# Performance work log

Hardware: AMD Instinct MI355X
Metric: run time of the kernel (lower is better)

Reference implementation:

```python
import jax, jax.numpy as jnp
import numpy as np
from jax import lax

B = 32      # point clouds per batch
P = 1024    # points per cloud (equal-sized, contiguous in batch vector)
K = 20      # kNN neighbors (includes self, as in PyG knn)
N = B * P


def _w(key, fan_in, fan_out):
    return jax.random.normal(key, (fan_in, fan_out), dtype=jnp.float32) / np.sqrt(fan_in)


def setup_inputs() -> dict:
    key = jax.random.key(0)
    ks = jax.random.split(key, 12)
    return {
        "pos": jax.random.normal(ks[0], (N, 3), dtype=jnp.float32),
        "batch": jnp.repeat(jnp.arange(B, dtype=jnp.int32), P),
        # conv1 MLP([6,64,64]): Linear(6,64)+BN+ReLU, Linear(64,64) plain
        "conv1_W1": _w(ks[1], 6, 64),
        "conv1_b1": jnp.zeros((64,), jnp.float32),
        "conv1_bn_scale": jnp.ones((64,), jnp.float32),   # BN eval folded affine
        "conv1_bn_bias": jnp.zeros((64,), jnp.float32),
        "conv1_W2": _w(ks[2], 64, 64),
        "conv1_b2": jnp.zeros((64,), jnp.float32),
        # conv2 MLP([128,128]): single plain Linear(128,128)
        "conv2_W": _w(ks[3], 128, 128),
        "conv2_b": jnp.zeros((128,), jnp.float32),
        # lin: Linear(64+128, 128)
        "lin_W": _w(ks[4], 192, 128),
        "lin_b": jnp.zeros((128,), jnp.float32),
    }


def _edge_conv(x, mlp_fn):
    # x: [B, P, d]. Dynamic kNN in feature space per cloud, edge MLP, max-aggregate.
    sq = jnp.sum(x * x, axis=-1)                                  # [B,P]
    dist = sq[:, :, None] - 2.0 * jnp.einsum('bpd,bqd->bpq', x, x) + sq[:, None, :]
    _, idx = lax.top_k(-dist, K)                                  # [B,P,K] nearest (incl. self)
    x_j = jax.vmap(lambda xb, ib: xb[ib])(x, idx)                 # [B,P,K,d] gather neighbors
    x_i = jnp.broadcast_to(x[:, :, None, :], x_j.shape)
    e = jnp.concatenate([x_i, x_j - x_i], axis=-1)                # [B,P,K,2d]
    return jnp.max(mlp_fn(e), axis=2)                             # max aggregation -> [B,P,out]


def reference(pos, batch, conv1_W1, conv1_b1, conv1_bn_scale, conv1_bn_bias,
              conv1_W2, conv1_b2, conv2_W, conv2_b, lin_W, lin_b):
    x = pos.reshape(B, P, 3)

    def mlp1(e):
        h = e @ conv1_W1 + conv1_b1
        h = jax.nn.relu(h * conv1_bn_scale + conv1_bn_bias)       # BN(eval) + ReLU
        return h @ conv1_W2 + conv1_b2                            # plain last layer

    def mlp2(e):
        return e @ conv2_W + conv2_b                              # plain single layer

    x1 = _edge_conv(x, mlp1)                                      # [B,P,64]
    x2 = _edge_conv(x1, mlp2)                                     # [B,P,128]
    h = jnp.concatenate([x1, x2], axis=-1) @ lin_W + lin_b        # [B,P,128]
    # global_max_pool over each cloud via batch ids
    out = jax.ops.segment_max(h.reshape(N, 128), batch, num_segments=B)
    return out                                                    # [B,128]
```

## Files before the change

kernel.cpp:

```cpp
#include <hip/hip_runtime.h>
#include <math.h>

#define NPTS 32768
#define NB 32
#define PP 1024
#define KK 20

using bf16x8 = __attribute__((ext_vector_type(8))) short;
using f32x4 = __attribute__((ext_vector_type(4))) float;

constexpr size_t OFF_X1 = 0;
constexpr size_t OFF_IDX = OFF_X1 + (size_t)NPTS * 64 * 4;
constexpr size_t OFF_U = OFF_IDX + (size_t)NPTS * KK * 4;
constexpr size_t OFF_V = OFF_U + (size_t)NPTS * 128 * 4;
constexpr size_t OFF_X2 = OFF_V + (size_t)NPTS * 128 * 4;
constexpr size_t OFF_H = OFF_X2 + (size_t)NPTS * 128 * 4;
constexpr size_t OFF_PART = OFF_H + (size_t)NPTS * 128 * 4;
constexpr size_t OFF_SQN = OFF_PART + (size_t)32 * 8 * 128 * 4;

__device__ __forceinline__ void topk_insert(unsigned (&l)[KK], unsigned key) {
#pragma unroll
  for (int j = KK - 1; j >= 1; --j) {
    unsigned r;
    asm("v_med3_u32 %0, %1, %2, %3" : "=v"(r) : "v"(key), "v"(l[j - 1]), "v"(l[j]));
    l[j] = r;
  }
  l[0] = key < l[0] ? key : l[0];
}

__device__ __forceinline__ unsigned pack_key(float dist, int q) {
  return (__float_as_uint(dist) & 0xFFFFFC00u) | (unsigned)q;
}

__device__ __forceinline__ void split_bf16(float x, short& hi, short& lo) {
  unsigned u = __float_as_uint(x);
  hi = (short)(u >> 16);
  float fh = __uint_as_float(u & 0xFFFF0000u);
  float r = x - fh;
  lo = (short)(__float_as_uint(r) >> 16);
}

template <int S>
__global__ __launch_bounds__(256, 4) void knn_topk3(const float* __restrict__ x,
                                                    unsigned* __restrict__ pk) {
  constexpr int CH = PP / S;
  __shared__ __align__(16) float xs[1024];
  __shared__ __align__(16) float ys[1024];
  __shared__ __align__(16) float zs[1024];
  int bx = blockIdx.x;
  int s = bx % S;
  int tile = (bx / S) % (PP / 256);
  int b = bx / (S * (PP / 256));
  int tid = threadIdx.x;
  const float* xb = x + (size_t)b * PP * 3;

  for (int t = tid; t < 768; t += 256) {
    float4 v = ((const float4*)xb)[t];
    int e = 4 * t;
    float vals[4] = {v.x, v.y, v.z, v.w};
#pragma unroll
    for (int j = 0; j < 4; ++j) {
      int p = (e + j) / 3, d = (e + j) % 3;
      if (d == 0) xs[p] = vals[j];
      else if (d == 1) ys[p] = vals[j];
      else zs[p] = vals[j];
    }
  }
  __syncthreads();

  int i = tile * 256 + tid;
  float xi0 = xs[i], xi1 = ys[i], xi2 = zs[i];

  unsigned l[KK];
#pragma unroll
  for (int j = 0; j < KK; ++j) l[j] = 0xFFFFFFFFu;

  int q0 = s * CH;
  float4 qx = *(const float4*)&xs[q0];
  float4 qy = *(const float4*)&ys[q0];
  float4 qz = *(const float4*)&zs[q0];
  for (int c = 0; c < CH; c += 4) {
    int qm = (q0 + c + 4) & 1023;
    float4 nqx = *(const float4*)&xs[qm];
    float4 nqy = *(const float4*)&ys[qm];
    float4 nqz = *(const float4*)&zs[qm];
    float cx[4] = {qx.x, qx.y, qx.z, qx.w};
    float cy[4] = {qy.x, qy.y, qy.z, qy.w};
    float cz[4] = {qz.x, qz.y, qz.z, qz.w};
#pragma unroll
    for (int j = 0; j < 4; ++j) {
      float d0 = xi0 - cx[j], d1 = xi1 - cy[j], d2 = xi2 - cz[j];
      float dist = fmaf(d0, d0, fmaf(d1, d1, d2 * d2));
      topk_insert(l, pack_key(dist, q0 + c + j));
    }
    qx = nqx; qy = nqy; qz = nqz;
  }
  size_t base = ((size_t)b * PP + i) * S + s;
#pragma unroll
  for (int j = 0; j < KK; ++j) pk[base * KK + j] = l[j];
}

template <int S>
__global__ __launch_bounds__(256) void knn_merge(const unsigned* __restrict__ pk,
                                                 int* __restrict__ idx_out) {
  int p = blockIdx.x * 256 + threadIdx.x;
  const unsigned* g = pk + (size_t)p * S * KK;
  unsigned l[KK];
#pragma unroll
  for (int j = 0; j < KK; ++j) l[j] = g[j];
  for (int s = 1; s < S; ++s) {
    const unsigned* gs = g + s * KK;
    for (int j = 0; j < KK; ++j) {
      unsigned key = gs[j];
      if (key >= l[KK - 1]) break;
      topk_insert(l, key);
    }
  }
#pragma unroll
  for (int j = 0; j < KK; ++j) idx_out[(size_t)p * KK + j] = (int)(l[j] & 1023u);
}

__global__ __launch_bounds__(256) void precompute1(const float* __restrict__ pos,
                                                   const float* __restrict__ W1,
                                                   const float* __restrict__ b1,
                                                   float* __restrict__ u1,
                                                   float* __restrict__ v1) {
  int gid = blockIdx.x * 256 + threadIdx.x;
  int i = gid >> 6, c = gid & 63;
  float p0 = pos[(size_t)i * 3 + 0], p1 = pos[(size_t)i * 3 + 1], p2 = pos[(size_t)i * 3 + 2];
  float a0 = W1[0 * 64 + c], a1 = W1[1 * 64 + c], a2 = W1[2 * 64 + c];
  float g0 = W1[3 * 64 + c], g1 = W1[4 * 64 + c], g2 = W1[5 * 64 + c];
  float v = fmaf(p0, g0, fmaf(p1, g1, p2 * g2));
  float u = b1[c];
  u = fmaf(p0, a0 - g0, u);
  u = fmaf(p1, a1 - g1, u);
  u = fmaf(p2, a2 - g2, u);
  u1[gid] = u;
  v1[gid] = v;
}

__global__ __launch_bounds__(256) void edge_conv1_mfma(
    const float* __restrict__ u1, const float* __restrict__ v1,
    const int* __restrict__ idx, const float* __restrict__ W2,
    const float* __restrict__ scale, const float* __restrict__ bias,
    const float* __restrict__ b2,
    short* __restrict__ x1hl, float* __restrict__ sqn) {
  __shared__ float Cs[160 * 68];
  __shared__ int jt[160];
  __shared__ float xs[512];
  int tid = threadIdx.x;
  int p0 = blockIdx.x * 8;
  int b = p0 >> 10;
  if (tid < 160) {
    int e = tid;
    int i = p0 + e / 20;
    jt[e] = (b << 10) + idx[(size_t)i * KK + e % 20];
  }
  int w = tid >> 6, l = tid & 63, quad = l >> 4, lm = l & 15;
  int kq = quad * 8;
  float4 s00 = *(const float4*)(scale + kq);
  float4 s01 = *(const float4*)(scale + kq + 4);
  float4 s10 = *(const float4*)(scale + 32 + kq);
  float4 s11 = *(const float4*)(scale + 32 + kq + 4);
  float4 c00 = *(const float4*)(bias + kq);
  float4 c01 = *(const float4*)(bias + kq + 4);
  float4 c10 = *(const float4*)(bias + 32 + kq);
  float4 c11 = *(const float4*)(bias + 32 + kq + 4);
  bf16x8 Bh[4][2], Bl[4][2];
#pragma unroll
  for (int nt = 0; nt < 4; ++nt) {
#pragma unroll
    for (int ks = 0; ks < 2; ++ks) {
#pragma unroll
      for (int jj = 0; jj < 8; ++jj) {
        float wv = W2[(size_t)(ks * 32 + kq + jj) * 64 + nt * 16 + lm];
        short hi, lo;
        split_bf16(wv, hi, lo);
        Bh[nt][ks][jj] = hi;
        Bl[nt][ks][jj] = lo;
      }
    }
  }
  __syncthreads();

  for (int s = w; s < 10; s += 4) {
    f32x4 acc[4];
#pragma unroll
    for (int nt = 0; nt < 4; ++nt) acc[nt] = (f32x4){0.f, 0.f, 0.f, 0.f};
    int e = s * 16 + lm;
    int p = e / 20;
    int jrow = jt[e];
    const float* urow = u1 + (size_t)(p0 + p) * 64;
    const float* vrow = v1 + (size_t)jrow * 64;
#pragma unroll
    for (int ks = 0; ks < 2; ++ks) {
      int koff = ks * 32 + kq;
      float4 va = *(const float4*)(vrow + koff);
      float4 vb = *(const float4*)(vrow + koff + 4);
      float4 ua = *(const float4*)(urow + koff);
      float4 ub = *(const float4*)(urow + koff + 4);
      float4 sA = ks ? s10 : s00, sB = ks ? s11 : s01;
      float4 cA = ks ? c10 : c00, cB = ks ? c11 : c01;
      float hv[8];
      hv[0] = fmaxf(fmaf(ua.x + va.x, sA.x, cA.x), 0.f);
      hv[1] = fmaxf(fmaf(ua.y + va.y, sA.y, cA.y), 0.f);
      hv[2] = fmaxf(fmaf(ua.z + va.z, sA.z, cA.z), 0.f);
      hv[3] = fmaxf(fmaf(ua.w + va.w, sA.w, cA.w), 0.f);
      hv[4] = fmaxf(fmaf(ub.x + vb.x, sB.x, cB.x), 0.f);
      hv[5] = fmaxf(fmaf(ub.y + vb.y, sB.y, cB.y), 0.f);
      hv[6] = fmaxf(fmaf(ub.z + vb.z, sB.z, cB.z), 0.f);
      hv[7] = fmaxf(fmaf(ub.w + vb.w, sB.w, cB.w), 0.f);
      bf16x8 Ah, Al;
#pragma unroll
      for (int jj = 0; jj < 8; ++jj) {
        short hi, lo;
        split_bf16(hv[jj], hi, lo);
        Ah[jj] = hi;
        Al[jj] = lo;
      }
#pragma unroll
      for (int nt = 0; nt < 4; ++nt) {
        acc[nt] = __builtin_amdgcn_mfma_f32_16x16x32_bf16(Ah, Bh[nt][ks], acc[nt], 0, 0, 0);
        acc[nt] = __builtin_amdgcn_mfma_f32_16x16x32_bf16(Al, Bh[nt][ks], acc[nt], 0, 0, 0);
        acc[nt] = __builtin_amdgcn_mfma_f32_16x16x32_bf16(Ah, Bl[nt][ks], acc[nt], 0, 0, 0);
      }
    }
#pragma unroll
    for (int nt = 0; nt < 4; ++nt) {
#pragma unroll
      for (int r = 0; r < 4; ++r) {
        Cs[(size_t)(s * 16 + quad * 4 + r) * 68 + nt * 16 + lm] = acc[nt][r];
      }
    }
  }
  __syncthreads();
  for (int o = tid; o < 512; o += 256) {
    int p = o >> 6, c = o & 63;
    float m = -__builtin_inff();
    for (int k = 0; k < KK; ++k) m = fmaxf(m, Cs[(size_t)(p * 20 + k) * 68 + c]);
    m += b2[c];
    size_t gi = (size_t)(p0 + p) * 128 + c;
    short hi, lo;
    split_bf16(m, hi, lo);
    x1hl[gi] = hi;
    x1hl[gi + 64] = lo;
    xs[o] = m;
  }
  __syncthreads();
  if (tid < 8) {
    float ss = 0.f;
    for (int c = 0; c < 64; ++c) {
      float v = xs[tid * 64 + c];
      ss = fmaf(v, v, ss);
    }
    sqn[p0 + tid] = ss;
  }
}

__global__ __launch_bounds__(256, 4) void knn2_mfma(const short* __restrict__ x1hl,
                                                    const float* __restrict__ sqn,
                                                    unsigned* __restrict__ pk) {
  constexpr int TS = 72;
  __shared__ float sqs[512];
  __shared__ __align__(16) short tileH[2][64 * TS];
  __shared__ __align__(16) short tileL[2][64 * TS];
  int bx = blockIdx.x;
  int s = bx & 1;
  int pb = bx >> 1;
  int p0 = pb * 64;
  int b = p0 >> 10;
  int tid = threadIdx.x;
  for (int t = tid; t < 512; t += 256) sqs[t] = sqn[(size_t)b * PP + s * 512 + t];
  int w = tid >> 6, l = tid & 63, quad = l >> 4, lm = l & 15;
  size_t gi = (size_t)p0 + w * 16 + lm;
  const short* brow = x1hl + gi * 128 + quad * 8;
  bf16x8 Bh0 = *(const bf16x8*)(brow);
  bf16x8 Bl0 = *(const bf16x8*)(brow + 64);
  bf16x8 Bh1 = *(const bf16x8*)(brow + 32);
  bf16x8 Bl1 = *(const bf16x8*)(brow + 96);
  float sqi = sqn[gi];

  unsigned la[KK], lc[KK];
#pragma unroll
  for (int j = 0; j < KK; ++j) { la[j] = 0xFFFFFFFFu; lc[j] = 0xFFFFFFFFu; }

  int rr = tid & 63, seg = tid >> 6;
  const short* srcbase = x1hl + ((size_t)b * PP + s * 512 + rr) * 128 + seg * 32;
  {
    bf16x8 r0 = *(const bf16x8*)(srcbase);
    bf16x8 r1 = *(const bf16x8*)(srcbase + 8);
    bf16x8 r2 = *(const bf16x8*)(srcbase + 16);
    bf16x8 r3 = *(const bf16x8*)(srcbase + 24);
    short* dst = ((seg < 2) ? tileH[0] : tileL[0]) + rr * TS + (seg & 1) * 32;
    *(bf16x8*)(dst) = r0;
    *(bf16x8*)(dst + 8) = r1;
    *(bf16x8*)(dst + 16) = r2;
    *(bf16x8*)(dst + 24) = r3;
  }
  __syncthreads();

  for (int tile = 0; tile < 8; ++tile) {
    int buf = tile & 1;
    bf16x8 r0, r1, r2, r3;
    if (tile < 7) {
      const short* src = srcbase + (size_t)(tile + 1) * 64 * 128;
      r0 = *(const bf16x8*)(src);
      r1 = *(const bf16x8*)(src + 8);
      r2 = *(const bf16x8*)(src + 16);
      r3 = *(const bf16x8*)(src + 24);
    }
#pragma unroll
    for (int it = 0; it < 4; ++it) {
      int row = it * 16 + lm;
      const short* aH = tileH[buf] + row * TS + quad * 8;
      const short* aL = tileL[buf] + row * TS + quad * 8;
      bf16x8 Ah0 = *(const bf16x8*)(aH);
      bf16x8 Ah1 = *(const bf16x8*)(aH + 32);
      bf16x8 Al0 = *(const bf16x8*)(aL);
      bf16x8 Al1 = *(const bf16x8*)(aL + 32);

      f32x4 acc = (f32x4){0.f, 0.f, 0.f, 0.f};
      acc = __builtin_amdgcn_mfma_f32_16x16x32_bf16(Ah0, Bh0, acc, 0, 0, 0);
      acc = __builtin_amdgcn_mfma_f32_16x16x32_bf16(Al0, Bh0, acc, 0, 0, 0);
      acc = __builtin_amdgcn_mfma_f32_16x16x32_bf16(Ah0, Bl0, acc, 0, 0, 0);
      acc = __builtin_amdgcn_mfma_f32_16x16x32_bf16(Ah1, Bh1, acc, 0, 0, 0);
      acc = __builtin_amdgcn_mfma_f32_16x16x32_bf16(Al1, Bh1, acc, 0, 0, 0);
      acc = __builtin_amdgcn_mfma_f32_16x16x32_bf16(Ah1, Bl1, acc, 0, 0, 0);

      int qloc = tile * 64 + it * 16 + quad * 4;
      int qg = s * 512 + qloc;
      float d0 = fmaxf(0.f, fmaf(-2.f, acc[0], sqi + sqs[qloc + 0]));
      float d2 = fmaxf(0.f, fmaf(-2.f, acc[2], sqi + sqs[qloc + 2]));
      topk_insert(la, pack_key(d0, qg + 0));
      topk_insert(lc, pack_key(d2, qg + 2));
      float d1 = fmaxf(0.f, fmaf(-2.f, acc[1], sqi + sqs[qloc + 1]));
      float d3 = fmaxf(0.f, fmaf(-2.f, acc[3], sqi + sqs[qloc + 3]));
      topk_insert(la, pack_key(d1, qg + 1));
      topk_insert(lc, pack_key(d3, qg + 3));
    }
    if (tile < 7) {
      __syncthreads();
      short* dst = ((seg < 2) ? tileH[buf ^ 1] : tileL[buf ^ 1]) + rr * TS + (seg & 1) * 32;
      *(bf16x8*)(dst) = r0;
      *(bf16x8*)(dst + 8) = r1;
      *(bf16x8*)(dst + 16) = r2;
      *(bf16x8*)(dst + 24) = r3;
      __syncthreads();
    }
  }
  for (int j = 0; j < KK; ++j) {
    unsigned key = lc[j];
    if (key >= la[KK - 1]) break;
    topk_insert(la, key);
  }
  unsigned sub = (unsigned)(s * 4 + quad);
  unsigned* dst = pk + ((size_t)gi * 8 + sub) * KK;
#pragma unroll
  for (int j = 0; j < KK; ++j) dst[j] = la[j];
}

__global__ __launch_bounds__(256) void pre2_mfma(const short* __restrict__ x1hl,
                                                 const float* __restrict__ cW,
                                                 const float* __restrict__ cb,
                                                 float* __restrict__ u2,
                                                 float* __restrict__ v2) {
  constexpr int BS = 72;
  __shared__ short Bh[128 * BS];
  __shared__ short Bl[128 * BS];
  int tid = threadIdx.x;
  int nh = blockIdx.x & 1;
  int p0 = (blockIdx.x >> 1) * 64;
  for (int t = tid; t < 64 * 128; t += 256) {
    int k = t >> 7, n = t & 127;
    float wb_ = cW[(size_t)(64 + k) * 128 + n];
    float wv = nh ? wb_ : (cW[(size_t)k * 128 + n] - wb_);
    short hi, lo;
    split_bf16(wv, hi, lo);
    Bh[n * BS + k] = hi;
    Bl[n * BS + k] = lo;
  }
  __syncthreads();
  int w = tid >> 6, l = tid & 63, quad = l >> 4, lm = l & 15;
  int row = p0 + w * 16 + lm;
  f32x4 acc[8];
#pragma unroll
  for (int nt = 0; nt < 8; ++nt) acc[nt] = (f32x4){0.f, 0.f, 0.f, 0.f};
#pragma unroll
  for (int ks = 0; ks < 2; ++ks) {
    int kb = ks * 32 + quad * 8;
    bf16x8 Ah = *(const bf16x8*)(x1hl + (size_t)row * 128 + kb);
    bf16x8 Al = *(const bf16x8*)(x1hl + (size_t)row * 128 + 64 + kb);
#pragma unroll
    for (int nt = 0; nt < 8; ++nt) {
      bf16x8 Wh = *(const bf16x8*)(Bh + (nt * 16 + lm) * BS + kb);
      bf16x8 Wl = *(const bf16x8*)(Bl + (nt * 16 + lm) * BS + kb);
      acc[nt] = __builtin_amdgcn_mfma_f32_16x16x32_bf16(Ah, Wh, acc[nt], 0, 0, 0);
      acc[nt] = __builtin_amdgcn_mfma_f32_16x16x32_bf16(Al, Wh, acc[nt], 0, 0, 0);
      acc[nt] = __builtin_amdgcn_mfma_f32_16x16x32_bf16(Ah, Wl, acc[nt], 0, 0, 0);
    }
  }
  float* out = nh ? v2 : u2;
  int prow = p0 + w * 16 + quad * 4;
#pragma unroll
  for (int nt = 0; nt < 8; ++nt) {
    int col = nt * 16 + lm;
    float bias = nh ? 0.f : cb[col];
#pragma unroll
    for (int r = 0; r < 4; ++r)
      out[(size_t)(prow + r) * 128 + col] = acc[nt][r] + bias;
  }
}

__global__ __launch_bounds__(256) void gathermax2(const float* __restrict__ u2,
                                                  const float* __restrict__ v2,
                                                  const int* __restrict__ idx,
                                                  short* __restrict__ x2hl) {
  int gid = blockIdx.x * 256 + threadIdx.x;
  int i = gid >> 7, c = gid & 127;
  int b = i >> 10;
  const int* myidx = idx + (size_t)i * KK;
  float m = -__builtin_inff();
  for (int k = 0; k < KK; ++k) {
    int j = (b << 10) + myidx[k];
    m = fmaxf(m, v2[(size_t)j * 128 + c]);
  }
  float x = u2[gid] + m;
  short hi, lo;
  split_bf16(x, hi, lo);
  x2hl[(size_t)i * 256 + c] = hi;
  x2hl[(size_t)i * 256 + 128 + c] = lo;
}

__global__ __launch_bounds__(256) void lin_mfma(const short* __restrict__ x1hl,
                                                const short* __restrict__ x2hl,
                                                const float* __restrict__ LW,
                                                const float* __restrict__ lb,
                                                float* __restrict__ h) {
  constexpr int BS = 200;
  __shared__ short Bh[64 * BS];
  __shared__ short Bl[64 * BS];
  int tid = threadIdx.x;
  int nh = blockIdx.x & 1;
  int p0 = (blockIdx.x >> 1) * 64;
  for (int t = tid; t < 192 * 64; t += 256) {
    int k = t >> 6, n = t & 63;
    float wv = LW[(size_t)k * 128 + nh * 64 + n];
    short hi, lo;
    split_bf16(wv, hi, lo);
    Bh[n * BS + k] = hi;
    Bl[n * BS + k] = lo;
  }
  __syncthreads();
  int w = tid >> 6, l = tid & 63, quad = l >> 4, lm = l & 15;
  int row = p0 + w * 16 + lm;
  f32x4 acc[4];
#pragma unroll
  for (int nt = 0; nt < 4; ++nt) acc[nt] = (f32x4){0.f, 0.f, 0.f, 0.f};
#pragma unroll
  for (int ks = 0; ks < 6; ++ks) {
    int kb = ks * 32 + quad * 8;
    bf16x8 Ah, Al;
    if (ks < 2) {
      Ah = *(const bf16x8*)(x1hl + (size_t)row * 128 + kb);
      Al = *(const bf16x8*)(x1hl + (size_t)row * 128 + 64 + kb);
    } else {
      Ah = *(const bf16x8*)(x2hl + (size_t)row * 256 + (kb - 64));
      Al = *(const bf16x8*)(x2hl + (size_t)row * 256 + 128 + (kb - 64));
    }
#pragma unroll
    for (int nt = 0; nt < 4; ++nt) {
      bf16x8 Wh = *(const bf16x8*)(Bh + (nt * 16 + lm) * BS + kb);
      bf16x8 Wl = *(const bf16x8*)(Bl + (nt * 16 + lm) * BS + kb);
      acc[nt] = __builtin_amdgcn_mfma_f32_16x16x32_bf16(Ah, Wh, acc[nt], 0, 0, 0);
      acc[nt] = __builtin_amdgcn_mfma_f32_16x16x32_bf16(Al, Wh, acc[nt], 0, 0, 0);
      acc[nt] = __builtin_amdgcn_mfma_f32_16x16x32_bf16(Ah, Wl, acc[nt], 0, 0, 0);
    }
  }
  int prow = p0 + w * 16 + quad * 4;
#pragma unroll
  for (int nt = 0; nt < 4; ++nt) {
    int col = nh * 64 + nt * 16 + lm;
    float bias = lb[col];
#pragma unroll
    for (int r = 0; r < 4; ++r)
      h[(size_t)(prow + r) * 128 + col] = acc[nt][r] + bias;
  }
}

__global__ __launch_bounds__(128) void segmax_a(const float* __restrict__ h,
                                                float* __restrict__ part) {
  int b = blockIdx.x >> 3, chunk = blockIdx.x & 7;
  int c = threadIdx.x;
  float m = -__builtin_inff();
  for (int p = 0; p < 128; ++p) {
    size_t i = (size_t)b * PP + chunk * 128 + p;
    m = fmaxf(m, h[i * 128 + c]);
  }
  part[(size_t)blockIdx.x * 128 + c] = m;
}

__global__ __launch_bounds__(128) void segmax_b(const float* __restrict__ part,
                                                float* __restrict__ out) {
  int b = blockIdx.x;
  int c = threadIdx.x;
  float m = -__builtin_inff();
  for (int k = 0; k < 8; ++k) m = fmaxf(m, part[((size_t)b * 8 + k) * 128 + c]);
  out[(size_t)b * 128 + c] = m;
}

extern "C" void kernel_launch(void* const* d_in, const int* in_sizes, int n_in,
                              void* d_out, int out_size, void* d_ws, size_t ws_size,
                              hipStream_t stream) {
  const float* pos = (const float*)d_in[0];
  const float* W1 = (const float*)d_in[2];
  const float* b1 = (const float*)d_in[3];
  const float* bn_s = (const float*)d_in[4];
  const float* bn_b = (const float*)d_in[5];
  const float* W2 = (const float*)d_in[6];
  const float* b2 = (const float*)d_in[7];
  const float* cW = (const float*)d_in[8];
  const float* cb = (const float*)d_in[9];
  const float* LW = (const float*)d_in[10];
  const float* lb = (const float*)d_in[11];
  float* out = (float*)d_out;

  char* ws = (char*)d_ws;
  short* x1hl = (short*)(ws + OFF_X1);
  int* idx = (int*)(ws + OFF_IDX);
  float* u1 = (float*)(ws + OFF_U);
  float* v1 = (float*)(ws + OFF_V);
  float* u2 = (float*)(ws + OFF_U);
  float* v2 = (float*)(ws + OFF_V);
  short* x2hl = (short*)(ws + OFF_X2);
  float* hbuf = (float*)(ws + OFF_H);
  float* part = (float*)(ws + OFF_PART);
  float* sqn = (float*)(ws + OFF_SQN);
  unsigned* pk = (unsigned*)(ws + OFF_U);

  knn_topk3<8><<<NB * 4 * 8, 256, 0, stream>>>(pos, pk);
  knn_merge<8><<<NPTS / 256, 256, 0, stream>>>(pk, idx);
  precompute1<<<NPTS * 64 / 256, 256, 0, stream>>>(pos, W1, b1, u1, v1);
  edge_conv1_mfma<<<NPTS / 8, 256, 0, stream>>>(u1, v1, idx, W2, bn_s, bn_b, b2,
                                                x1hl, sqn);
  knn2_mfma<<<NPTS / 64 * 2, 256, 0, stream>>>(x1hl, sqn, pk);
  knn_merge<8><<<NPTS / 256, 256, 0, stream>>>(pk, idx);
  pre2_mfma<<<NPTS / 64 * 2, 256, 0, stream>>>(x1hl, cW, cb, u2, v2);
  gathermax2<<<NPTS * 128 / 256, 256, 0, stream>>>(u2, v2, idx, x2hl);
  lin_mfma<<<NPTS / 64 * 2, 256, 0, stream>>>(x1hl, x2hl, LW, lb, hbuf);
  segmax_a<<<NB * 8, 128, 0, stream>>>(hbuf, part);
  segmax_b<<<NB, 128, 0, stream>>>(part, out);
}
```

Measured before the change: 341.5 us.

## Restructure edge_conv1 so MFMA rows are points and max-reduce in registers

The edge_conv1 kernel now handles 32 points per block instead of 8. Each MFMA row corresponds to one point, and each wave pair splits that point's 20 neighbors in half. The max over neighbors is kept in registers, which removes the large shared-memory edge buffer and its serial 20-way reduction loop. The u*scale+bias term is precomputed once per point so each edge needs only one FMA, and the W2 bf16 split is amortized over four times more points per block. The change trades grid size (4x fewer blocks) for less LDS traffic and fewer redundant loads.

```diff
diff --git a/kernel.cpp b/kernel.cpp
--- a/kernel.cpp
+++ b/kernel.cpp
@@ -145,27 +145,16 @@
     const float* __restrict__ scale, const float* __restrict__ bias,
     const float* __restrict__ b2,
     short* __restrict__ x1hl, float* __restrict__ sqn) {
-  __shared__ float Cs[160 * 68];
-  __shared__ int jt[160];
-  __shared__ float xs[512];
+  __shared__ int jt[32 * KK];
+  __shared__ float mxs[32 * 68];
   int tid = threadIdx.x;
-  int p0 = blockIdx.x * 8;
+  int p0 = blockIdx.x * 32;
   int b = p0 >> 10;
-  if (tid < 160) {
-    int e = tid;
-    int i = p0 + e / 20;
-    jt[e] = (b << 10) + idx[(size_t)i * KK + e % 20];
-  }
+  for (int t = tid; t < 32 * KK; t += 256)
+    jt[t] = (b << 10) + idx[(size_t)(p0 + t / KK) * KK + t % KK];
   int w = tid >> 6, l = tid & 63, quad = l >> 4, lm = l & 15;
+  int group = w >> 1, khalf = w & 1;
   int kq = quad * 8;
-  float4 s00 = *(const float4*)(scale + kq);
-  float4 s01 = *(const float4*)(scale + kq + 4);
-  float4 s10 = *(const float4*)(scale + 32 + kq);
-  float4 s11 = *(const float4*)(scale + 32 + kq + 4);
-  float4 c00 = *(const float4*)(bias + kq);
-  float4 c01 = *(const float4*)(bias + kq + 4);
-  float4 c10 = *(const float4*)(bias + 32 + kq);
-  float4 c11 = *(const float4*)(bias + 32 + kq + 4);
   bf16x8 Bh[4][2], Bl[4][2];
 #pragma unroll
   for (int nt = 0; nt < 4; ++nt) {
@@ -181,35 +170,59 @@
       }
     }
   }
-  __syncthreads();
-
-  for (int s = w; s < 10; s += 4) {
+  int myp = group * 16 + lm;
+  const float* urow = u1 + (size_t)(p0 + myp) * 64;
+  float up[2][8], sc[2][8];
+#pragma unroll
+  for (int ks = 0; ks < 2; ++ks) {
+    int koff = ks * 32 + kq;
+    float4 ua = *(const float4*)(urow + koff);
+    float4 ub = *(const float4*)(urow + koff + 4);
+    float4 sa = *(const float4*)(scale + koff);
+    float4 sb = *(const float4*)(scale + koff + 4);
+    float4 ca = *(const float4*)(bias + koff);
+    float4 cb4 = *(const float4*)(bias + koff + 4);
+    sc[ks][0] = sa.x; sc[ks][1] = sa.y; sc[ks][2] = sa.z; sc[ks][3] = sa.w;
+    sc[ks][4] = sb.x; sc[ks][5] = sb.y; sc[ks][6] = sb.z; sc[ks][7] = sb.w;
+    up[ks][0] = fmaf(ua.x, sa.x, ca.x);
+    up[ks][1] = fmaf(ua.y, sa.y, ca.y);
+    up[ks][2] = fmaf(ua.z, sa.z, ca.z);
+    up[ks][3] = fmaf(ua.w, sa.w, ca.w);
+    up[ks][4] = fmaf(ub.x, sb.x, cb4.x);
+    up[ks][5] = fmaf(ub.y, sb.y, cb4.y);
+    up[ks][6] = fmaf(ub.z, sb.z, cb4.z);
+    up[ks][7] = fmaf(ub.w, sb.w, cb4.w);
+  }
+  float b2v[4];
+#pragma unroll
+  for (int nt = 0; nt < 4; ++nt) b2v[nt] = b2[nt * 16 + lm];
+  __syncthreads();
+
+  f32x4 mx[4];
+#pragma unroll
+  for (int nt = 0; nt < 4; ++nt)
+    mx[nt] = (f32x4){-__builtin_inff(), -__builtin_inff(), -__builtin_inff(), -__builtin_inff()};
+
+  for (int k = khalf * 10; k < khalf * 10 + 10; ++k) {
+    int j = jt[myp * KK + k];
+    const float* vrow = v1 + (size_t)j * 64;
     f32x4 acc[4];
 #pragma unroll
     for (int nt = 0; nt < 4; ++nt) acc[nt] = (f32x4){0.f, 0.f, 0.f, 0.f};
-    int e = s * 16 + lm;
-    int p = e / 20;
-    int jrow = jt[e];
-    const float* urow = u1 + (size_t)(p0 + p) * 64;
-    const float* vrow = v1 + (size_t)jrow * 64;
 #pragma unroll
     for (int ks = 0; ks < 2; ++ks) {
       int koff = ks * 32 + kq;
       float4 va = *(const float4*)(vrow + koff);
       float4 vb = *(const float4*)(vrow + koff + 4);
-      float4 ua = *(const float4*)(urow + koff);
-      float4 ub = *(const float4*)(urow + koff + 4);
-      float4 sA = ks ? s10 : s00, sB = ks ? s11 : s01;
-      float4 cA = ks ? c10 : c00, cB = ks ? c11 : c01;
       float hv[8];
-      hv[0] = fmaxf(fmaf(ua.x + va.x, sA.x, cA.x), 0.f);
-      hv[1] = fmaxf(fmaf(ua.y + va.y, sA.y, cA.y), 0.f);
-      hv[2] = fmaxf(fmaf(ua.z + va.z, sA.z, cA.z), 0.f);
-      hv[3] = fmaxf(fmaf(ua.w + va.w, sA.w, cA.w), 0.f);
-      hv[4] = fmaxf(fmaf(ub.x + vb.x, sB.x, cB.x), 0.f);
-      hv[5] = fmaxf(fmaf(ub.y + vb.y, sB.y, cB.y), 0.f);
-      hv[6] = fmaxf(fmaf(ub.z + vb.z, sB.z, cB.z), 0.f);
-      hv[7] = fmaxf(fmaf(ub.w + vb.w, sB.w, cB.w), 0.f);
+      hv[0] = fmaxf(fmaf(va.x, sc[ks][0], up[ks][0]), 0.f);
+      hv[1] = fmaxf(fmaf(va.y, sc[ks][1], up[ks][1]), 0.f);
+      hv[2] = fmaxf(fmaf(va.z, sc[ks][2], up[ks][2]), 0.f);
+      hv[3] = fmaxf(fmaf(va.w, sc[ks][3], up[ks][3]), 0.f);
+      hv[4] = fmaxf(fmaf(vb.x, sc[ks][4], up[ks][4]), 0.f);
+      hv[5] = fmaxf(fmaf(vb.y, sc[ks][5], up[ks][5]), 0.f);
+      hv[6] = fmaxf(fmaf(vb.z, sc[ks][6], up[ks][6]), 0.f);
+      hv[7] = fmaxf(fmaf(vb.w, sc[ks][7], up[ks][7]), 0.f);
       bf16x8 Ah, Al;
 #pragma unroll
       for (int jj = 0; jj < 8; ++jj) {
@@ -228,29 +241,39 @@
 #pragma unroll
     for (int nt = 0; nt < 4; ++nt) {
 #pragma unroll
+      for (int r = 0; r < 4; ++r) mx[nt][r] = fmaxf(mx[nt][r], acc[nt][r]);
+    }
+  }
+  if (khalf == 1) {
+#pragma unroll
+    for (int nt = 0; nt < 4; ++nt)
+#pragma unroll
+      for (int r = 0; r < 4; ++r)
+        mxs[(group * 16 + quad * 4 + r) * 68 + nt * 16 + lm] = mx[nt][r];
+  }
+  __syncthreads();
+  if (khalf == 0) {
+#pragma unroll
+    for (int nt = 0; nt < 4; ++nt) {
+#pragma unroll
       for (int r = 0; r < 4; ++r) {
-        Cs[(size_t)(s * 16 + quad * 4 + r) * 68 + nt * 16 + lm] = acc[nt][r];
+        int p = group * 16 + quad * 4 + r;
+        int c = nt * 16 + lm;
+        float m = fmaxf(mx[nt][r], mxs[p * 68 + c]) + b2v[nt];
+        short hi, lo;
+        split_bf16(m, hi, lo);
+        size_t gi = (size_t)(p0 + p) * 128 + c;
+        x1hl[gi] = hi;
+        x1hl[gi + 64] = lo;
+        mxs[p * 68 + c] = m;
       }
     }
   }
   __syncthreads();
-  for (int o = tid; o < 512; o += 256) {
-    int p = o >> 6, c = o & 63;
-    float m = -__builtin_inff();
-    for (int k = 0; k < KK; ++k) m = fmaxf(m, Cs[(size_t)(p * 20 + k) * 68 + c]);
-    m += b2[c];
-    size_t gi = (size_t)(p0 + p) * 128 + c;
-    short hi, lo;
-    split_bf16(m, hi, lo);
-    x1hl[gi] = hi;
-    x1hl[gi + 64] = lo;
-    xs[o] = m;
-  }
-  __syncthreads();
-  if (tid < 8) {
+  if (tid < 32) {
     float ss = 0.f;
     for (int c = 0; c < 64; ++c) {
-      float v = xs[tid * 64 + c];
+      float v = mxs[tid * 68 + c];
       ss = fmaf(v, v, ss);
     }
     sqn[p0 + tid] = ss;
@@ -540,8 +563,8 @@
   knn_topk3<8><<<NB * 4 * 8, 256, 0, stream>>>(pos, pk);
   knn_merge<8><<<NPTS / 256, 256, 0, stream>>>(pk, idx);
   precompute1<<<NPTS * 64 / 256, 256, 0, stream>>>(pos, W1, b1, u1, v1);
-  edge_conv1_mfma<<<NPTS / 8, 256, 0, stream>>>(u1, v1, idx, W2, bn_s, bn_b, b2,
-                                                x1hl, sqn);
+  edge_conv1_mfma<<<NPTS / 32, 256, 0, stream>>>(u1, v1, idx, W2, bn_s, bn_b, b2,
+                                                 x1hl, sqn);
   knn2_mfma<<<NPTS / 64 * 2, 256, 0, stream>>>(x1hl, sqn, pk);
   knn_merge<8><<<NPTS / 256, 256, 0, stream>>>(pk, idx);
   pre2_mfma<<<NPTS / 64 * 2, 256, 0, stream>>>(x1hl, cW, cb, u2, v2);
```

Result: no change. 335.2 us (-1.8%).
